# Kernel tuning notes

Hardware: AMD Instinct MI355X
Metric: run time of the kernel (lower is better)

The kernel has to match this reference:

```python
import jax, jax.numpy as jnp
import numpy as np
from jax import lax

B, N, C = 8, 16384, 128
HEADS, FF, KS = 8, 3.0, 5
HD = C // HEADS

def setup_inputs() -> dict:
    key = jax.random.key(0)
    ks = jax.random.split(key, 10)
    r = lambda k, s, sc=0.02: jax.random.normal(k, s, dtype=jnp.float32) * sc
    return {
        "x": jax.random.normal(ks[0], (B, N, C), dtype=jnp.float32),
        "Wq": r(ks[1], (C, C)),
        "Wkv": r(ks[2], (C, C)),
        "Wproj": r(ks[3], (C, C)),
        "bproj": jnp.zeros((C,), jnp.float32),
        "w_g": jax.random.normal(ks[4], (C, 1), dtype=jnp.float32),
        "scale": r(ks[5], (1, 1, C), 0.1),
        "pos_enc": r(ks[6], (1, N, C), 0.02),
        "dwc_w": r(ks[7], (HD, 1, KS, KS), 0.1),
        "dwc_b": jnp.zeros((HD,), jnp.float32),
        "H": 128,
        "W": 128,
    }

def _l2(a, axis):
    return jnp.sqrt(jnp.sum(a * a, axis=axis, keepdims=True))

def reference(x, Wq, Wkv, Wproj, bproj, w_g, scale, pos_enc, dwc_w, dwc_b, H, W):
    b, n_tok, c = x.shape
    scale_factor = HD ** (-0.5)
    q = x @ Wq.T                      # (B,N,C)
    k = x @ Wkv.T + pos_enc           # (B,N,C)  sr_ratio=1 path
    s = jax.nn.softplus(scale)
    q = (jax.nn.relu(q) + 1e-6) / s
    k = (jax.nn.relu(k) + 1e-6) / s
    qn, kn = _l2(q, -1), _l2(k, -1)
    q = q ** FF
    k = k ** FF
    q = q / _l2(q, -1) * qn
    k = k / _l2(k, -1) * kn
    A = (q @ w_g) * scale_factor      # (B,N,1)
    A = A / jnp.maximum(_l2(A, 1), 1e-12)  # F.normalize over dim=1
    G = jnp.sum(A * q, axis=1)        # (B,C)
    xg = G[:, None, :] * k            # (B,N,C)
    qh = q.reshape(b, n_tok, HEADS, HD).transpose(0, 2, 1, 3)  # (B,h,N,d)
    kh = k.reshape(b, n_tok, HEADS, HD).transpose(0, 2, 1, 3)
    z = 1.0 / (jnp.einsum('bhnd,bhd->bhn', qh, kh.mean(axis=2)) + 1e-6)
    xh = xg.reshape(b, n_tok, HEADS, HD).transpose(0, 2, 1, 3) * z[..., None]
    xo = xh.transpose(0, 2, 1, 3).reshape(b, n_tok, c)
    # faithful second transpose+reshape (memory reinterpretation in the source)
    xo = xo.transpose(0, 2, 1).reshape(b, n_tok, c)
    kimg = kh.reshape(b * HEADS, H, W, HD).transpose(0, 3, 1, 2)  # (B*h,d,H,W)
    pad = KS // 2
    conv = lax.conv_general_dilated(kimg, dwc_w, (1, 1), [(pad, pad), (pad, pad)],
                                    dimension_numbers=('NCHW', 'OIHW', 'NCHW'),
                                    feature_group_count=HD)
    conv = conv + dwc_b[None, :, None, None]
    xo = xo + conv.reshape(b, c, n_tok).transpose(0, 2, 1)
    return xo @ Wproj.T + bproj
```

## Files before the change

### kernel.cpp

```cpp
#include <hip/hip_runtime.h>
#include <hip/hip_bf16.h>

#define BB 8
#define NN 16384
#define CC 128

typedef __attribute__((ext_vector_type(8))) short bf16x8;
typedef __attribute__((ext_vector_type(4))) short short4v;
typedef __attribute__((ext_vector_type(4))) float f32x4;

__device__ __forceinline__ unsigned short f2bf(float f) {
    union { float f; unsigned u; } v; v.f = f;
    unsigned r = v.u + 0x7fffu + ((v.u >> 16) & 1u);
    return (unsigned short)(r >> 16);
}
__device__ __forceinline__ float bf2f(unsigned short h) {
    union { unsigned u; float f; } v; v.u = ((unsigned)h) << 16;
    return v.f;
}
__device__ __forceinline__ void split_trunc(float f, short& hi, short& lo) {
    union { float f; unsigned u; } v; v.f = f;
    const unsigned short hu = (unsigned short)(v.u >> 16);
    union { unsigned u; float f; } hf; hf.u = ((unsigned)hu) << 16;
    union { float f; unsigned u; } r; r.f = f - hf.f;
    hi = (short)hu;
    lo = (short)(r.u >> 16);
}

__global__ __launch_bounds__(256) void wprep_kernel(
    const float* __restrict__ Wq, const float* __restrict__ Wkv,
    const float* __restrict__ Wp, const float* __restrict__ scale,
    unsigned short* __restrict__ whi, unsigned short* __restrict__ wlo,
    float* __restrict__ sps)
{
    const int bid = blockIdx.x;
    if (bid == 48) {
        if (threadIdx.x < 128)
            sps[threadIdx.x] = 1.f / log1pf(expf(scale[threadIdx.x]));
        return;
    }
    const int mat = bid >> 4;
    const float* src = (mat == 0) ? Wq : ((mat == 1) ? Wkv : Wp);
    const int off = (bid & 15) * 1024 + threadIdx.x * 4;
    const float4 v = *(const float4*)(src + off);
    float f[4] = {v.x, v.y, v.z, v.w};
    short4v hv, lv;
#pragma unroll
    for (int j = 0; j < 4; ++j) {
        short h, lo2;
        split_trunc(f[j], h, lo2);
        hv[j] = h; lv[j] = lo2;
    }
    *(short4v*)(whi + mat * 16384 + off) = hv;
    *(short4v*)(wlo + mat * 16384 + off) = lv;
}

__global__ __launch_bounds__(256, 1) void qk_mfma_kernel(
    const float* __restrict__ x, const unsigned short* __restrict__ whi,
    const unsigned short* __restrict__ wlo, const float* __restrict__ w_g,
    const float* __restrict__ sps, const float* __restrict__ pos_enc,
    unsigned short* __restrict__ qout, unsigned short* __restrict__ ktout,
    float* __restrict__ partial)
{
    __shared__ __align__(16) char wsm[131072];
    __shared__ float wpart[4][257];
    __shared__ float apl[128];

    const int tid  = threadIdx.x;
    const int w    = tid >> 6;
    const int l    = tid & 63;
    const int blk  = blockIdx.x;
    const int tok0 = blk * 128;
    const int tokb = (blk & 127) * 128;

    bf16x8 xh[2][4], xl[2][4];
#pragma unroll
    for (int n = 0; n < 2; ++n) {
        const int r = w * 32 + n * 16 + (l & 15);
        const float* rowp = x + (tok0 + r) * 128 + (l >> 4) * 8;
#pragma unroll
        for (int kt = 0; kt < 4; ++kt) {
            const f32x4 a = *(const f32x4*)(rowp + kt * 32);
            const f32x4 b = *(const f32x4*)(rowp + kt * 32 + 4);
            const float f[8] = {a[0], a[1], a[2], a[3], b[0], b[1], b[2], b[3]};
            bf16x8 hv, lv;
#pragma unroll
            for (int j = 0; j < 8; ++j) {
                short h, lo2;
                split_trunc(f[j], h, lo2);
                hv[j] = h; lv[j] = lo2;
            }
            xh[n][kt] = hv; xl[n][kt] = lv;
        }
    }

#pragma unroll
    for (int it = 0; it < 32; ++it) {
        const int flat = it * 256 + tid;
        const int arr  = flat >> 11;
        const int c    = (flat >> 4) & 127;
        const int g    = flat & 15;
        const unsigned short* src = ((arr & 1) ? wlo : whi)
                                  + ((arr >> 1) ? 16384 : 0) + c * 128 + g * 8;
        const int dst = arr * 32768 + c * 256 + ((g * 16) ^ ((c & 7) << 4));
        *(bf16x8*)(wsm + dst) = *(const bf16x8*)src;
    }
    __syncthreads();

    const int crow = (l >> 4) * 4;
    f32x4 accq[8][2], acck[8][2];
#pragma unroll
    for (int m = 0; m < 8; ++m)
#pragma unroll
        for (int n = 0; n < 2; ++n) { accq[m][n] = (f32x4)0.f; acck[m][n] = (f32x4)0.f; }

#pragma unroll
    for (int m = 0; m < 8; ++m) {
        const int c = m * 16 + (l & 15);
        const int sw = (c & 7) << 4;
        bf16x8 aqh[4], aql[4], akh[4], akl[4];
#pragma unroll
        for (int kt = 0; kt < 4; ++kt) {
            const int fo = c * 256 + ((kt * 64 + (l >> 4) * 16) ^ sw);
            aqh[kt] = *(const bf16x8*)(wsm + fo);
            aql[kt] = *(const bf16x8*)(wsm + 32768 + fo);
            akh[kt] = *(const bf16x8*)(wsm + 65536 + fo);
            akl[kt] = *(const bf16x8*)(wsm + 98304 + fo);
        }
#pragma unroll
        for (int n = 0; n < 2; ++n)
#pragma unroll
            for (int kt = 0; kt < 4; ++kt) {
                accq[m][n] = __builtin_amdgcn_mfma_f32_16x16x32_bf16(aqh[kt], xh[n][kt], accq[m][n], 0, 0, 0);
                acck[m][n] = __builtin_amdgcn_mfma_f32_16x16x32_bf16(akh[kt], xh[n][kt], acck[m][n], 0, 0, 0);
                accq[m][n] = __builtin_amdgcn_mfma_f32_16x16x32_bf16(aqh[kt], xl[n][kt], accq[m][n], 0, 0, 0);
                acck[m][n] = __builtin_amdgcn_mfma_f32_16x16x32_bf16(akh[kt], xl[n][kt], acck[m][n], 0, 0, 0);
                accq[m][n] = __builtin_amdgcn_mfma_f32_16x16x32_bf16(aql[kt], xh[n][kt], accq[m][n], 0, 0, 0);
                acck[m][n] = __builtin_amdgcn_mfma_f32_16x16x32_bf16(akl[kt], xh[n][kt], acck[m][n], 0, 0, 0);
            }
    }
    __syncthreads();

    {
#pragma unroll
        for (int m = 0; m < 8; ++m) {
            const float4 is4 = *(const float4*)(sps + m * 16 + crow);
            const float is[4] = {is4.x, is4.y, is4.z, is4.w};
#pragma unroll
            for (int n = 0; n < 2; ++n)
#pragma unroll
                for (int j = 0; j < 4; ++j)
                    accq[m][n][j] = (fmaxf(accq[m][n][j], 0.f) + 1e-6f) * is[j];
        }
        float fqn[2];
#pragma unroll
        for (int n = 0; n < 2; ++n) {
            float s2 = 0.f, s6 = 0.f;
#pragma unroll
            for (int m = 0; m < 8; ++m)
#pragma unroll
                for (int j = 0; j < 4; ++j) {
                    const float v = accq[m][n][j], v2 = v * v;
                    s2 += v2; s6 += v2 * v2 * v2;
                }
            s2 += __shfl_xor(s2, 16); s6 += __shfl_xor(s6, 16);
            s2 += __shfl_xor(s2, 32); s6 += __shfl_xor(s6, 32);
            fqn[n] = sqrtf(s2 / s6);
        }
#pragma unroll
        for (int m = 0; m < 8; ++m)
#pragma unroll
            for (int n = 0; n < 2; ++n)
#pragma unroll
                for (int j = 0; j < 4; ++j) {
                    const float v = accq[m][n][j];
                    accq[m][n][j] = v * v * v * fqn[n];
                }
        float d0 = 0.f, d1 = 0.f;
#pragma unroll
        for (int m = 0; m < 8; ++m) {
            const float4 wgv = *(const float4*)(w_g + m * 16 + crow);
#pragma unroll
            for (int j = 0; j < 4; ++j) {
                const float wg = (j == 0) ? wgv.x : (j == 1) ? wgv.y : (j == 2) ? wgv.z : wgv.w;
                d0 += accq[m][0][j] * wg;
                d1 += accq[m][1][j] * wg;
            }
        }
        d0 += __shfl_xor(d0, 16); d0 += __shfl_xor(d0, 32);
        d1 += __shfl_xor(d1, 16); d1 += __shfl_xor(d1, 32);
        const float ap0 = 0.25f * d0, ap1 = 0.25f * d1;

        float ssa = ap0 * ap0 + ap1 * ap1;
        ssa += __shfl_xor(ssa, 1); ssa += __shfl_xor(ssa, 2);
        ssa += __shfl_xor(ssa, 4); ssa += __shfl_xor(ssa, 8);
        if (l == 0) wpart[w][256] = ssa;
        if (l < 16) { apl[w * 32 + l] = ap0; apl[w * 32 + 16 + l] = ap1; }

        float g4[4] = {0.f, 0.f, 0.f, 0.f};
#pragma unroll
        for (int n = 0; n < 2; ++n) {
            const int t = l & 15;
            const int rb = w * 8192 + t * 512;
#pragma unroll
            for (int m = 0; m < 8; ++m) {
                const int ad = rb + (((m * 16 + crow) * 4) ^ ((t & 7) << 4));
                *(f32x4*)(wsm + ad) = accq[m][n];
            }
            asm volatile("s_waitcnt lgkmcnt(0)" ::: "memory");
#pragma unroll
            for (int j = 0; j < 8; ++j) {
                const int fid = j * 64 + l;
                const int row = fid >> 5;
                const int c4  = fid & 31;
                const int rb3 = w * 8192 + row * 512;
                const f32x4 v = *(f32x4*)(wsm + rb3 + ((c4 * 16) ^ ((row & 7) << 4)));
                const float apv = apl[w * 32 + n * 16 + row];
                short4v qv;
#pragma unroll
                for (int i = 0; i < 4; ++i) {
                    g4[i] += apv * v[i];
                    qv[i] = (short)f2bf(v[i]);
                }
                *(short4v*)(qout + (tok0 + w * 32 + n * 16 + row) * 128 + c4 * 4) = qv;
            }
        }
#pragma unroll
        for (int i = 0; i < 4; ++i) g4[i] += __shfl_xor(g4[i], 32);
        if (l < 32) {
#pragma unroll
            for (int i = 0; i < 4; ++i) wpart[w][(l & 31) * 4 + i] = g4[i];
        }
    }

    {
#pragma unroll
        for (int m = 0; m < 8; ++m) {
            const float4 is4 = *(const float4*)(sps + m * 16 + crow);
            const float is[4] = {is4.x, is4.y, is4.z, is4.w};
#pragma unroll
            for (int n = 0; n < 2; ++n) {
                const int t = tokb + w * 32 + n * 16 + (l & 15);
                const float4 p = *(const float4*)(pos_enc + t * 128 + m * 16 + crow);
                const float pe[4] = {p.x, p.y, p.z, p.w};
#pragma unroll
                for (int j = 0; j < 4; ++j)
                    acck[m][n][j] = (fmaxf(acck[m][n][j] + pe[j], 0.f) + 1e-6f) * is[j];
            }
        }
        float fkn[2];
#pragma unroll
        for (int n = 0; n < 2; ++n) {
            float s2 = 0.f, s6 = 0.f;
#pragma unroll
            for (int m = 0; m < 8; ++m)
#pragma unroll
                for (int j = 0; j < 4; ++j) {
                    const float v = acck[m][n][j], v2 = v * v;
                    s2 += v2; s6 += v2 * v2 * v2;
                }
            s2 += __shfl_xor(s2, 16); s6 += __shfl_xor(s6, 16);
            s2 += __shfl_xor(s2, 32); s6 += __shfl_xor(s6, 32);
            fkn[n] = sqrtf(s2 / s6);
        }
#pragma unroll
        for (int m = 0; m < 8; ++m)
#pragma unroll
            for (int n = 0; n < 2; ++n)
#pragma unroll
                for (int j = 0; j < 4; ++j) {
                    const float v = acck[m][n][j];
                    acck[m][n][j] = v * v * v * fkn[n];
                }
#pragma unroll
        for (int m = 0; m < 8; ++m)
#pragma unroll
            for (int j = 0; j < 4; ++j) {
                float s = acck[m][0][j] + acck[m][1][j];
                s += __shfl_xor(s, 1); s += __shfl_xor(s, 2);
                s += __shfl_xor(s, 4); s += __shfl_xor(s, 8);
                if ((l & 15) == 0) wpart[w][128 + m * 16 + crow + j] = s;
            }
    }

    __syncthreads();
#pragma unroll
    for (int m = 0; m < 8; ++m)
#pragma unroll
        for (int n = 0; n < 2; ++n)
#pragma unroll
            for (int j = 0; j < 4; ++j) {
                const int ch = m * 16 + crow + j;
                const int tl = w * 32 + n * 16 + (l & 15);
                *(unsigned short*)(wsm + ch * 264 + tl * 2) = f2bf(acck[m][n][j]);
            }
    __syncthreads();
    {
        const int bb = blk >> 7;
        unsigned* ktp = (unsigned*)ktout;
#pragma unroll
        for (int it = 0; it < 32; ++it) {
            const int idx = it * 256 + tid;
            const int row = idx >> 6;
            const int col = idx & 63;
            const unsigned v = *(unsigned*)(wsm + row * 264 + col * 4);
            ktp[(size_t)(bb * 128 + row) * 8192 + (blk & 127) * 64 + col] = v;
        }
    }

    __syncthreads();
    float* pblk = partial + blk * 257;
    if (tid < 128) {
        pblk[tid] = wpart[0][tid] + wpart[1][tid] + wpart[2][tid] + wpart[3][tid];
        pblk[128 + tid] = wpart[0][128 + tid] + wpart[1][128 + tid] +
                          wpart[2][128 + tid] + wpart[3][128 + tid];
    } else if (tid == 128) {
        pblk[256] = wpart[0][256] + wpart[1][256] + wpart[2][256] + wpart[3][256];
    }
}

__global__ __launch_bounds__(256) void reduce_kernel(
    const float* __restrict__ partial, float* __restrict__ G,
    float* __restrict__ kbar)
{
    const int b = blockIdx.x;
    const int tid = threadIdx.x;
    __shared__ float tmp[4];

    float ssa = (tid < 128) ? partial[(b * 128 + tid) * 257 + 256] : 0.f;
#pragma unroll
    for (int o = 32; o >= 1; o >>= 1) ssa += __shfl_xor(ssa, o);
    if ((tid & 63) == 0) tmp[tid >> 6] = ssa;
    __syncthreads();
    const float anorm = fmaxf(sqrtf(tmp[0] + tmp[1] + tmp[2] + tmp[3]), 1e-12f);
    const float inv_a = 1.f / anorm;

    if (tid < 128) {
        float g = 0.f;
        for (int t = 0; t < 128; ++t)
            g += partial[(b * 128 + t) * 257 + tid];
        G[b * 128 + tid] = g * inv_a;
    } else {
        const int c2 = tid - 128;
        float s = 0.f;
        for (int t = 0; t < 128; ++t)
            s += partial[(b * 128 + t) * 257 + 128 + c2];
        kbar[b * 128 + c2] = s * (1.f / 16384.f);
    }
}

__global__ __launch_bounds__(256) void z_kernel(
    const unsigned short* __restrict__ q, const float* __restrict__ kbar,
    float* __restrict__ z)
{
    const int bid = blockIdx.x;
    const int b   = bid >> 8;
    const int tg  = bid & 255;
    const int tid = threadIdx.x;
    const int t   = tid >> 2;
    const int qt  = tid & 3;
    const int tok = tg * 64 + t;

    const unsigned short* qp = q + ((size_t)b * NN + tok) * 128 + qt * 32;
    const float* kb = kbar + b * 128 + qt * 32;

    float dot0 = 0.f, dot1 = 0.f;
#pragma unroll
    for (int c = 0; c < 4; ++c) {
        const short4v q4a = *(const short4v*)(qp + c * 8);
        const short4v q4b = *(const short4v*)(qp + c * 8 + 4);
        const float4 k4a = *(const float4*)(kb + c * 8);
        const float4 k4b = *(const float4*)(kb + c * 8 + 4);
        float d = bf2f((unsigned short)q4a[0]) * k4a.x + bf2f((unsigned short)q4a[1]) * k4a.y +
                  bf2f((unsigned short)q4a[2]) * k4a.z + bf2f((unsigned short)q4a[3]) * k4a.w +
                  bf2f((unsigned short)q4b[0]) * k4b.x + bf2f((unsigned short)q4b[1]) * k4b.y +
                  bf2f((unsigned short)q4b[2]) * k4b.z + bf2f((unsigned short)q4b[3]) * k4b.w;
        if (c < 2) dot0 += d; else dot1 += d;
    }
    z[((size_t)b * 8 + qt * 2) * NN + tok]     = 1.f / (dot0 + 1e-6f);
    z[((size_t)b * 8 + qt * 2 + 1) * NN + tok] = 1.f / (dot1 + 1e-6f);
}

__global__ __launch_bounds__(256, 2) void scp_kernel(
    float* __restrict__ out, const unsigned short* __restrict__ kt,
    const float* __restrict__ z, const float* __restrict__ G,
    const unsigned short* __restrict__ whi, const unsigned short* __restrict__ wlo,
    const float* __restrict__ bp, const float* __restrict__ dwc_w,
    const float* __restrict__ dwc_b)
{
    __shared__ __align__(16) char smem[32768];
    __shared__ float wct[25][16];
    __shared__ float bi[16];
    __shared__ float Gs;

    const int tid  = threadIdx.x;
    const int bid0 = blockIdx.x;
    const int bid  = (bid0 & 7) * 128 + (bid0 >> 3);
    const int cc   = bid & 127;
    const int b    = bid >> 7;
    const int n0   = bid * 128;

    for (int i = tid; i < 400; i += 256)
        wct[i >> 4][i & 15] = dwc_w[(i & 15) * 25 + (i >> 4)];
    if (tid < 16) bi[tid] = dwc_b[tid];
    if (tid == 0) Gs = G[b * 128 + cc];
    __syncthreads();

    const int ch4 = tid >> 3;
    const int xg  = tid & 7;

    float acc[4][16];
#pragma unroll
    for (int c = 0; c < 4; ++c)
#pragma unroll
        for (int i = 0; i < 16; ++i) acc[c][i] = 0.f;

#pragma unroll
    for (int dy = 0; dy < 5; ++dy) {
        const int yy = cc + dy - 2;
        if (yy < 0 || yy > 127) continue;
#pragma unroll
        for (int c = 0; c < 4; ++c) {
            const int ch = ch4 * 4 + c;
            const unsigned short* rowp = kt + ((size_t)b * 128 + ch) * NN
                                            + yy * 128 + xg * 16 - 8;
            float wf[32];
#pragma unroll
            for (int q4 = 0; q4 < 4; ++q4) {
                const bf16x8 v = *(const bf16x8*)(rowp + q4 * 8);
#pragma unroll
                for (int e = 0; e < 8; ++e)
                    wf[q4 * 8 + e] = bf2f((unsigned short)v[e]);
            }
            if (xg == 0) {
#pragma unroll
                for (int e = 0; e < 8; ++e) wf[e] = 0.f;
            }
            if (xg == 7) {
#pragma unroll
                for (int e = 24; e < 32; ++e) wf[e] = 0.f;
            }
            const int d = ch & 15;
#pragma unroll
            for (int dx = 0; dx < 5; ++dx) {
                const float wv = wct[dy * 5 + dx][d];
#pragma unroll
                for (int i = 0; i < 16; ++i)
                    acc[c][i] += wv * wf[i + dx + 6];
            }
        }
    }

    const float Gcc = Gs;
    const unsigned short* kub = kt + ((size_t)b * 128 + cc) * NN;
    const float* zr = z + ((size_t)b * 8 + (cc >> 4)) * NN;
    const int dbase = (ch4 & 3) * 4;
    const float4 b4 = *(const float4*)(&bi[dbase]);
    const float bv[4] = {b4.x, b4.y, b4.z, b4.w};
#pragma unroll
    for (int i = 0; i < 16; ++i) {
        const int r = xg * 16 + i;
        const int toks = r * 128 + ch4 * 4;
        const short4v ku4 = *(const short4v*)(kub + toks);
        const float4 z4 = *(const float4*)(zr + toks);
        const float zz[4] = {z4.x, z4.y, z4.z, z4.w};
        short4v hv;
#pragma unroll
        for (int c = 0; c < 4; ++c) {
            const float f = Gcc * bf2f((unsigned short)ku4[c]) * zz[c] + acc[c][i] + bv[c];
            hv[c] = (short)f2bf(f);
        }
        const int ad = r * 256 + (((ch4 >> 1) * 16) ^ ((r & 7) << 4)) + (ch4 & 1) * 8;
        *(short4v*)(smem + ad) = hv;
    }
    __syncthreads();

    const int w  = tid >> 6;
    const int ll = tid & 63;
    bf16x8 xh[2][4];
    {
        const int lg16 = (ll >> 4) * 16;
#pragma unroll
        for (int n = 0; n < 2; ++n) {
            const int r = w * 32 + n * 16 + (ll & 15);
            const int rb = r * 256;
            const int sw = (r & 7) << 4;
#pragma unroll
            for (int kt2 = 0; kt2 < 4; ++kt2)
                xh[n][kt2] = *(bf16x8*)(smem + rb + ((kt2 * 64 + lg16) ^ sw));
        }
    }
    const int crow = (ll >> 4) * 4;
    f32x4 pacc[8][2];
#pragma unroll
    for (int m = 0; m < 8; ++m)
#pragma unroll
        for (int n = 0; n < 2; ++n) pacc[m][n] = (f32x4)0.f;

#pragma unroll
    for (int m = 0; m < 8; ++m) {
        const int c = m * 16 + (ll & 15);
        bf16x8 ah[4], al[4];
#pragma unroll
        for (int kt2 = 0; kt2 < 4; ++kt2) {
            const int off = 32768 + c * 128 + kt2 * 32 + (ll >> 4) * 8;
            ah[kt2] = *(const bf16x8*)(whi + off);
            al[kt2] = *(const bf16x8*)(wlo + off);
        }
#pragma unroll
        for (int n = 0; n < 2; ++n)
#pragma unroll
            for (int kt2 = 0; kt2 < 4; ++kt2) {
                pacc[m][n] = __builtin_amdgcn_mfma_f32_16x16x32_bf16(ah[kt2], xh[n][kt2], pacc[m][n], 0, 0, 0);
                pacc[m][n] = __builtin_amdgcn_mfma_f32_16x16x32_bf16(al[kt2], xh[n][kt2], pacc[m][n], 0, 0, 0);
            }
    }

#pragma unroll
    for (int m = 0; m < 8; ++m) {
        const float4 bq = *(const float4*)(bp + m * 16 + crow);
        const float bb[4] = {bq.x, bq.y, bq.z, bq.w};
#pragma unroll
        for (int n = 0; n < 2; ++n)
#pragma unroll
            for (int j = 0; j < 4; ++j) pacc[m][n][j] += bb[j];
    }
    __syncthreads();
#pragma unroll
    for (int n = 0; n < 2; ++n) {
        const int t = ll & 15;
        const int rb = w * 8192 + t * 512;
#pragma unroll
        for (int m = 0; m < 8; ++m) {
            const int ad = rb + (((m * 16 + crow) * 4) ^ ((t & 7) << 4));
            *(f32x4*)(smem + ad) = pacc[m][n];
        }
        asm volatile("s_waitcnt lgkmcnt(0)" ::: "memory");
#pragma unroll
        for (int j = 0; j < 8; ++j) {
            const int fid = j * 64 + ll;
            const int row = fid >> 5;
            const int c4  = fid & 31;
            const int rb3 = w * 8192 + row * 512;
            const f32x4 v = *(f32x4*)(smem + rb3 + ((c4 * 16) ^ ((row & 7) << 4)));
            *(f32x4*)(out + (n0 + w * 32 + n * 16 + row) * 128 + c4 * 4) = v;
        }
    }
}

extern "C" void kernel_launch(void* const* d_in, const int* in_sizes, int n_in,
                              void* d_out, int out_size, void* d_ws, size_t ws_size,
                              hipStream_t stream)
{
    const float* x       = (const float*)d_in[0];
    const float* Wq      = (const float*)d_in[1];
    const float* Wkv     = (const float*)d_in[2];
    const float* Wproj   = (const float*)d_in[3];
    const float* bproj   = (const float*)d_in[4];
    const float* w_g     = (const float*)d_in[5];
    const float* scale   = (const float*)d_in[6];
    const float* pos_enc = (const float*)d_in[7];
    const float* dwc_w   = (const float*)d_in[8];
    const float* dwc_b   = (const float*)d_in[9];
    float* out = (float*)d_out;

    char* ws = (char*)d_ws;
    unsigned short* qbuf = (unsigned short*)(ws);
    unsigned short* ktbuf= (unsigned short*)(ws + 33554432);
    float* partial = (float*)(ws + 67108864);
    float* G       = (float*)(ws + 68161536);
    float* kbar    = (float*)(ws + 68165632);
    unsigned short* whi = (unsigned short*)(ws + 68169728);
    unsigned short* wlo = (unsigned short*)(ws + 68268032);
    float* sps     = (float*)(ws + 68366336);
    float* zbuf    = (float*)(ws + 68366848);

    wprep_kernel<<<dim3(49), dim3(256), 0, stream>>>(
        Wq, Wkv, Wproj, scale, whi, wlo, sps);
    qk_mfma_kernel<<<dim3(1024), dim3(256), 0, stream>>>(
        x, whi, wlo, w_g, sps, pos_enc, qbuf, ktbuf, partial);
    reduce_kernel<<<dim3(8), dim3(256), 0, stream>>>(partial, G, kbar);
    z_kernel<<<dim3(2048), dim3(256), 0, stream>>>(qbuf, kbar, zbuf);
    scp_kernel<<<dim3(1024), dim3(256), 0, stream>>>(
        out, ktbuf, zbuf, G, whi, wlo, bproj, dwc_w, dwc_b);
}
```

Baseline: 181.0 us.

## Split fused Q/K projection kernel into separate Q and K kernels

The single kernel that computed both Q and K projections, holding 128 KB of weights in LDS and two accumulator sets with one block per CU, is split into two kernels. Each loads only its own 64 KB of split-bf16 weights and has one accumulator set, and the launch bound allows two blocks per CU. The aim is higher occupancy and better latency hiding, at the price of reading and splitting x twice and paying an extra launch. The partial-sum buffers are separated and the reduce kernel is updated to match.

```diff
diff --git a/kernel.cpp b/kernel.cpp
--- a/kernel.cpp
+++ b/kernel.cpp
@@ -55,16 +55,189 @@
     *(short4v*)(wlo + mat * 16384 + off) = lv;
 }
 
-__global__ __launch_bounds__(256, 1) void qk_mfma_kernel(
+__global__ __launch_bounds__(256, 2) void qproj_kernel(
     const float* __restrict__ x, const unsigned short* __restrict__ whi,
     const unsigned short* __restrict__ wlo, const float* __restrict__ w_g,
+    const float* __restrict__ sps,
+    unsigned short* __restrict__ qout, float* __restrict__ partial1)
+{
+    __shared__ __align__(16) char wsm[65536];
+    __shared__ float wpart[4][132];
+    __shared__ float apl[128];
+
+    const int tid  = threadIdx.x;
+    const int w    = tid >> 6;
+    const int l    = tid & 63;
+    const int blk  = blockIdx.x;
+    const int tok0 = blk * 128;
+
+    bf16x8 xh[2][4], xl[2][4];
+#pragma unroll
+    for (int n = 0; n < 2; ++n) {
+        const int r = w * 32 + n * 16 + (l & 15);
+        const float* rowp = x + (tok0 + r) * 128 + (l >> 4) * 8;
+#pragma unroll
+        for (int kt = 0; kt < 4; ++kt) {
+            const f32x4 a = *(const f32x4*)(rowp + kt * 32);
+            const f32x4 b = *(const f32x4*)(rowp + kt * 32 + 4);
+            const float f[8] = {a[0], a[1], a[2], a[3], b[0], b[1], b[2], b[3]};
+            bf16x8 hv, lv;
+#pragma unroll
+            for (int j = 0; j < 8; ++j) {
+                short h, lo2;
+                split_trunc(f[j], h, lo2);
+                hv[j] = h; lv[j] = lo2;
+            }
+            xh[n][kt] = hv; xl[n][kt] = lv;
+        }
+    }
+
+#pragma unroll
+    for (int it = 0; it < 16; ++it) {
+        const int flat = it * 256 + tid;
+        const int arr  = flat >> 11;
+        const int c    = (flat >> 4) & 127;
+        const int g    = flat & 15;
+        const unsigned short* src = (arr ? wlo : whi) + c * 128 + g * 8;
+        const int dst = arr * 32768 + c * 256 + ((g * 16) ^ ((c & 7) << 4));
+        *(bf16x8*)(wsm + dst) = *(const bf16x8*)src;
+    }
+    __syncthreads();
+
+    const int crow = (l >> 4) * 4;
+    f32x4 acc[8][2];
+#pragma unroll
+    for (int m = 0; m < 8; ++m)
+#pragma unroll
+        for (int n = 0; n < 2; ++n) acc[m][n] = (f32x4)0.f;
+
+#pragma unroll
+    for (int m = 0; m < 8; ++m) {
+        const int c = m * 16 + (l & 15);
+        const int sw = (c & 7) << 4;
+        bf16x8 ah[4], al[4];
+#pragma unroll
+        for (int kt = 0; kt < 4; ++kt) {
+            const int fo = c * 256 + ((kt * 64 + (l >> 4) * 16) ^ sw);
+            ah[kt] = *(const bf16x8*)(wsm + fo);
+            al[kt] = *(const bf16x8*)(wsm + 32768 + fo);
+        }
+#pragma unroll
+        for (int n = 0; n < 2; ++n)
+#pragma unroll
+            for (int kt = 0; kt < 4; ++kt) {
+                acc[m][n] = __builtin_amdgcn_mfma_f32_16x16x32_bf16(ah[kt], xh[n][kt], acc[m][n], 0, 0, 0);
+                acc[m][n] = __builtin_amdgcn_mfma_f32_16x16x32_bf16(ah[kt], xl[n][kt], acc[m][n], 0, 0, 0);
+                acc[m][n] = __builtin_amdgcn_mfma_f32_16x16x32_bf16(al[kt], xh[n][kt], acc[m][n], 0, 0, 0);
+            }
+    }
+    __syncthreads();
+
+#pragma unroll
+    for (int m = 0; m < 8; ++m) {
+        const float4 is4 = *(const float4*)(sps + m * 16 + crow);
+        const float is[4] = {is4.x, is4.y, is4.z, is4.w};
+#pragma unroll
+        for (int n = 0; n < 2; ++n)
+#pragma unroll
+            for (int j = 0; j < 4; ++j)
+                acc[m][n][j] = (fmaxf(acc[m][n][j], 0.f) + 1e-6f) * is[j];
+    }
+    float fqn[2];
+#pragma unroll
+    for (int n = 0; n < 2; ++n) {
+        float s2 = 0.f, s6 = 0.f;
+#pragma unroll
+        for (int m = 0; m < 8; ++m)
+#pragma unroll
+            for (int j = 0; j < 4; ++j) {
+                const float v = acc[m][n][j], v2 = v * v;
+                s2 += v2; s6 += v2 * v2 * v2;
+            }
+        s2 += __shfl_xor(s2, 16); s6 += __shfl_xor(s6, 16);
+        s2 += __shfl_xor(s2, 32); s6 += __shfl_xor(s6, 32);
+        fqn[n] = sqrtf(s2 / s6);
+    }
+#pragma unroll
+    for (int m = 0; m < 8; ++m)
+#pragma unroll
+        for (int n = 0; n < 2; ++n)
+#pragma unroll
+            for (int j = 0; j < 4; ++j) {
+                const float v = acc[m][n][j];
+                acc[m][n][j] = v * v * v * fqn[n];
+            }
+    float d0 = 0.f, d1 = 0.f;
+#pragma unroll
+    for (int m = 0; m < 8; ++m) {
+        const float4 wgv = *(const float4*)(w_g + m * 16 + crow);
+#pragma unroll
+        for (int j = 0; j < 4; ++j) {
+            const float wg = (j == 0) ? wgv.x : (j == 1) ? wgv.y : (j == 2) ? wgv.z : wgv.w;
+            d0 += acc[m][0][j] * wg;
+            d1 += acc[m][1][j] * wg;
+        }
+    }
+    d0 += __shfl_xor(d0, 16); d0 += __shfl_xor(d0, 32);
+    d1 += __shfl_xor(d1, 16); d1 += __shfl_xor(d1, 32);
+    const float ap0 = 0.25f * d0, ap1 = 0.25f * d1;
+
+    float ssa = ap0 * ap0 + ap1 * ap1;
+    ssa += __shfl_xor(ssa, 1); ssa += __shfl_xor(ssa, 2);
+    ssa += __shfl_xor(ssa, 4); ssa += __shfl_xor(ssa, 8);
+    if (l == 0) wpart[w][128] = ssa;
+    if (l < 16) { apl[w * 32 + l] = ap0; apl[w * 32 + 16 + l] = ap1; }
+
+    float g4[4] = {0.f, 0.f, 0.f, 0.f};
+#pragma unroll
+    for (int n = 0; n < 2; ++n) {
+        const int t = l & 15;
+        const int rb = w * 8192 + t * 512;
+#pragma unroll
+        for (int m = 0; m < 8; ++m) {
+            const int ad = rb + (((m * 16 + crow) * 4) ^ ((t & 7) << 4));
+            *(f32x4*)(wsm + ad) = acc[m][n];
+        }
+        asm volatile("s_waitcnt lgkmcnt(0)" ::: "memory");
+#pragma unroll
+        for (int j = 0; j < 8; ++j) {
+            const int fid = j * 64 + l;
+            const int row = fid >> 5;
+            const int c4  = fid & 31;
+            const int rb3 = w * 8192 + row * 512;
+            const f32x4 v = *(f32x4*)(wsm + rb3 + ((c4 * 16) ^ ((row & 7) << 4)));
+            const float apv = apl[w * 32 + n * 16 + row];
+            short4v qv;
+#pragma unroll
+            for (int i = 0; i < 4; ++i) {
+                g4[i] += apv * v[i];
+                qv[i] = (short)f2bf(v[i]);
+            }
+            *(short4v*)(qout + (tok0 + w * 32 + n * 16 + row) * 128 + c4 * 4) = qv;
+        }
+    }
+#pragma unroll
+    for (int i = 0; i < 4; ++i) g4[i] += __shfl_xor(g4[i], 32);
+    if (l < 32) {
+#pragma unroll
+        for (int i = 0; i < 4; ++i) wpart[w][(l & 31) * 4 + i] = g4[i];
+    }
+    __syncthreads();
+    float* pblk = partial1 + blk * 132;
+    if (tid < 128)
+        pblk[tid] = wpart[0][tid] + wpart[1][tid] + wpart[2][tid] + wpart[3][tid];
+    else if (tid == 128)
+        pblk[128] = wpart[0][128] + wpart[1][128] + wpart[2][128] + wpart[3][128];
+}
+
+__global__ __launch_bounds__(256, 2) void kproj_kernel(
+    const float* __restrict__ x, const unsigned short* __restrict__ whi,
+    const unsigned short* __restrict__ wlo,
     const float* __restrict__ sps, const float* __restrict__ pos_enc,
-    unsigned short* __restrict__ qout, unsigned short* __restrict__ ktout,
-    float* __restrict__ partial)
+    unsigned short* __restrict__ ktout, float* __restrict__ partial2)
 {
-    __shared__ __align__(16) char wsm[131072];
-    __shared__ float wpart[4][257];
-    __shared__ float apl[128];
+    __shared__ __align__(16) char wsm[65536];
+    __shared__ float wpart[4][128];
 
     const int tid  = threadIdx.x;
     const int w    = tid >> 6;
@@ -95,195 +268,94 @@
     }
 
 #pragma unroll
-    for (int it = 0; it < 32; ++it) {
+    for (int it = 0; it < 16; ++it) {
         const int flat = it * 256 + tid;
         const int arr  = flat >> 11;
         const int c    = (flat >> 4) & 127;
         const int g    = flat & 15;
-        const unsigned short* src = ((arr & 1) ? wlo : whi)
-                                  + ((arr >> 1) ? 16384 : 0) + c * 128 + g * 8;
+        const unsigned short* src = (arr ? wlo : whi) + 16384 + c * 128 + g * 8;
         const int dst = arr * 32768 + c * 256 + ((g * 16) ^ ((c & 7) << 4));
         *(bf16x8*)(wsm + dst) = *(const bf16x8*)src;
     }
     __syncthreads();
 
     const int crow = (l >> 4) * 4;
-    f32x4 accq[8][2], acck[8][2];
+    f32x4 acc[8][2];
 #pragma unroll
     for (int m = 0; m < 8; ++m)
 #pragma unroll
-        for (int n = 0; n < 2; ++n) { accq[m][n] = (f32x4)0.f; acck[m][n] = (f32x4)0.f; }
+        for (int n = 0; n < 2; ++n) acc[m][n] = (f32x4)0.f;
 
 #pragma unroll
     for (int m = 0; m < 8; ++m) {
         const int c = m * 16 + (l & 15);
         const int sw = (c & 7) << 4;
-        bf16x8 aqh[4], aql[4], akh[4], akl[4];
+        bf16x8 ah[4], al[4];
 #pragma unroll
         for (int kt = 0; kt < 4; ++kt) {
             const int fo = c * 256 + ((kt * 64 + (l >> 4) * 16) ^ sw);
-            aqh[kt] = *(const bf16x8*)(wsm + fo);
-            aql[kt] = *(const bf16x8*)(wsm + 32768 + fo);
-            akh[kt] = *(const bf16x8*)(wsm + 65536 + fo);
-            akl[kt] = *(const bf16x8*)(wsm + 98304 + fo);
+            ah[kt] = *(const bf16x8*)(wsm + fo);
+            al[kt] = *(const bf16x8*)(wsm + 32768 + fo);
         }
 #pragma unroll
         for (int n = 0; n < 2; ++n)
 #pragma unroll
             for (int kt = 0; kt < 4; ++kt) {
-                accq[m][n] = __builtin_amdgcn_mfma_f32_16x16x32_bf16(aqh[kt], xh[n][kt], accq[m][n], 0, 0, 0);
-                acck[m][n] = __builtin_amdgcn_mfma_f32_16x16x32_bf16(akh[kt], xh[n][kt], acck[m][n], 0, 0, 0);
-                accq[m][n] = __builtin_amdgcn_mfma_f32_16x16x32_bf16(aqh[kt], xl[n][kt], accq[m][n], 0, 0, 0);
-                acck[m][n] = __builtin_amdgcn_mfma_f32_16x16x32_bf16(akh[kt], xl[n][kt], acck[m][n], 0, 0, 0);
-                accq[m][n] = __builtin_amdgcn_mfma_f32_16x16x32_bf16(aql[kt], xh[n][kt], accq[m][n], 0, 0, 0);
-                acck[m][n] = __builtin_amdgcn_mfma_f32_16x16x32_bf16(akl[kt], xh[n][kt], acck[m][n], 0, 0, 0);
-            }
-    }
-    __syncthreads();
-
-    {
-#pragma unroll
-        for (int m = 0; m < 8; ++m) {
-            const float4 is4 = *(const float4*)(sps + m * 16 + crow);
-            const float is[4] = {is4.x, is4.y, is4.z, is4.w};
-#pragma unroll
-            for (int n = 0; n < 2; ++n)
-#pragma unroll
-                for (int j = 0; j < 4; ++j)
-                    accq[m][n][j] = (fmaxf(accq[m][n][j], 0.f) + 1e-6f) * is[j];
-        }
-        float fqn[2];
+                acc[m][n] = __builtin_amdgcn_mfma_f32_16x16x32_bf16(ah[kt], xh[n][kt], acc[m][n], 0, 0, 0);
+                acc[m][n] = __builtin_amdgcn_mfma_f32_16x16x32_bf16(ah[kt], xl[n][kt], acc[m][n], 0, 0, 0);
+                acc[m][n] = __builtin_amdgcn_mfma_f32_16x16x32_bf16(al[kt], xh[n][kt], acc[m][n], 0, 0, 0);
+            }
+    }
+    __syncthreads();
+
+#pragma unroll
+    for (int m = 0; m < 8; ++m) {
+        const float4 is4 = *(const float4*)(sps + m * 16 + crow);
+        const float is[4] = {is4.x, is4.y, is4.z, is4.w};
 #pragma unroll
         for (int n = 0; n < 2; ++n) {
-            float s2 = 0.f, s6 = 0.f;
-#pragma unroll
-            for (int m = 0; m < 8; ++m)
-#pragma unroll
-                for (int j = 0; j < 4; ++j) {
-                    const float v = accq[m][n][j], v2 = v * v;
-                    s2 += v2; s6 += v2 * v2 * v2;
-                }
-            s2 += __shfl_xor(s2, 16); s6 += __shfl_xor(s6, 16);
-            s2 += __shfl_xor(s2, 32); s6 += __shfl_xor(s6, 32);
-            fqn[n] = sqrtf(s2 / s6);
-        }
+            const int t = tokb + w * 32 + n * 16 + (l & 15);
+            const float4 p = *(const float4*)(pos_enc + t * 128 + m * 16 + crow);
+            const float pe[4] = {p.x, p.y, p.z, p.w};
+#pragma unroll
+            for (int j = 0; j < 4; ++j)
+                acc[m][n][j] = (fmaxf(acc[m][n][j] + pe[j], 0.f) + 1e-6f) * is[j];
+        }
+    }
+    float fkn[2];
+#pragma unroll
+    for (int n = 0; n < 2; ++n) {
+        float s2 = 0.f, s6 = 0.f;
 #pragma unroll
         for (int m = 0; m < 8; ++m)
 #pragma unroll
-            for (int n = 0; n < 2; ++n)
-#pragma unroll
-                for (int j = 0; j < 4; ++j) {
-                    const float v = accq[m][n][j];
-                    accq[m][n][j] = v * v * v * fqn[n];
-                }
-        float d0 = 0.f, d1 = 0.f;
-#pragma unroll
-        for (int m = 0; m < 8; ++m) {
-            const float4 wgv = *(const float4*)(w_g + m * 16 + crow);
-#pragma unroll
             for (int j = 0; j < 4; ++j) {
-                const float wg = (j == 0) ? wgv.x : (j == 1) ? wgv.y : (j == 2) ? wgv.z : wgv.w;
-                d0 += accq[m][0][j] * wg;
-                d1 += accq[m][1][j] * wg;
-            }
-        }
-        d0 += __shfl_xor(d0, 16); d0 += __shfl_xor(d0, 32);
-        d1 += __shfl_xor(d1, 16); d1 += __shfl_xor(d1, 32);
-        const float ap0 = 0.25f * d0, ap1 = 0.25f * d1;
-
-        float ssa = ap0 * ap0 + ap1 * ap1;
-        ssa += __shfl_xor(ssa, 1); ssa += __shfl_xor(ssa, 2);
-        ssa += __shfl_xor(ssa, 4); ssa += __shfl_xor(ssa, 8);
-        if (l == 0) wpart[w][256] = ssa;
-        if (l < 16) { apl[w * 32 + l] = ap0; apl[w * 32 + 16 + l] = ap1; }
-
-        float g4[4] = {0.f, 0.f, 0.f, 0.f};
-#pragma unroll
-        for (int n = 0; n < 2; ++n) {
-            const int t = l & 15;
-            const int rb = w * 8192 + t * 512;
-#pragma unroll
-            for (int m = 0; m < 8; ++m) {
-                const int ad = rb + (((m * 16 + crow) * 4) ^ ((t & 7) << 4));
-                *(f32x4*)(wsm + ad) = accq[m][n];
-            }
-            asm volatile("s_waitcnt lgkmcnt(0)" ::: "memory");
-#pragma unroll
-            for (int j = 0; j < 8; ++j) {
-                const int fid = j * 64 + l;
-                const int row = fid >> 5;
-                const int c4  = fid & 31;
-                const int rb3 = w * 8192 + row * 512;
-                const f32x4 v = *(f32x4*)(wsm + rb3 + ((c4 * 16) ^ ((row & 7) << 4)));
-                const float apv = apl[w * 32 + n * 16 + row];
-                short4v qv;
-#pragma unroll
-                for (int i = 0; i < 4; ++i) {
-                    g4[i] += apv * v[i];
-                    qv[i] = (short)f2bf(v[i]);
-                }
-                *(short4v*)(qout + (tok0 + w * 32 + n * 16 + row) * 128 + c4 * 4) = qv;
-            }
-        }
-#pragma unroll
-        for (int i = 0; i < 4; ++i) g4[i] += __shfl_xor(g4[i], 32);
-        if (l < 32) {
-#pragma unroll
-            for (int i = 0; i < 4; ++i) wpart[w][(l & 31) * 4 + i] = g4[i];
-        }
-    }
-
-    {
-#pragma unroll
-        for (int m = 0; m < 8; ++m) {
-            const float4 is4 = *(const float4*)(sps + m * 16 + crow);
-            const float is[4] = {is4.x, is4.y, is4.z, is4.w};
-#pragma unroll
-            for (int n = 0; n < 2; ++n) {
-                const int t = tokb + w * 32 + n * 16 + (l & 15);
-                const float4 p = *(const float4*)(pos_enc + t * 128 + m * 16 + crow);
-                const float pe[4] = {p.x, p.y, p.z, p.w};
-#pragma unroll
-                for (int j = 0; j < 4; ++j)
-                    acck[m][n][j] = (fmaxf(acck[m][n][j] + pe[j], 0.f) + 1e-6f) * is[j];
-            }
-        }
-        float fkn[2];
-#pragma unroll
-        for (int n = 0; n < 2; ++n) {
-            float s2 = 0.f, s6 = 0.f;
-#pragma unroll
-            for (int m = 0; m < 8; ++m)
-#pragma unroll
-                for (int j = 0; j < 4; ++j) {
-                    const float v = acck[m][n][j], v2 = v * v;
-                    s2 += v2; s6 += v2 * v2 * v2;
-                }
-            s2 += __shfl_xor(s2, 16); s6 += __shfl_xor(s6, 16);
-            s2 += __shfl_xor(s2, 32); s6 += __shfl_xor(s6, 32);
-            fkn[n] = sqrtf(s2 / s6);
-        }
-#pragma unroll
-        for (int m = 0; m < 8; ++m)
-#pragma unroll
-            for (int n = 0; n < 2; ++n)
-#pragma unroll
-                for (int j = 0; j < 4; ++j) {
-                    const float v = acck[m][n][j];
-                    acck[m][n][j] = v * v * v * fkn[n];
-                }
-#pragma unroll
-        for (int m = 0; m < 8; ++m)
+                const float v = acc[m][n][j], v2 = v * v;
+                s2 += v2; s6 += v2 * v2 * v2;
+            }
+        s2 += __shfl_xor(s2, 16); s6 += __shfl_xor(s6, 16);
+        s2 += __shfl_xor(s2, 32); s6 += __shfl_xor(s6, 32);
+        fkn[n] = sqrtf(s2 / s6);
+    }
+#pragma unroll
+    for (int m = 0; m < 8; ++m)
+#pragma unroll
+        for (int n = 0; n < 2; ++n)
 #pragma unroll
             for (int j = 0; j < 4; ++j) {
-                float s = acck[m][0][j] + acck[m][1][j];
-                s += __shfl_xor(s, 1); s += __shfl_xor(s, 2);
-                s += __shfl_xor(s, 4); s += __shfl_xor(s, 8);
-                if ((l & 15) == 0) wpart[w][128 + m * 16 + crow + j] = s;
-            }
-    }
-
-    __syncthreads();
+                const float v = acc[m][n][j];
+                acc[m][n][j] = v * v * v * fkn[n];
+            }
+#pragma unroll
+    for (int m = 0; m < 8; ++m)
+#pragma unroll
+        for (int j = 0; j < 4; ++j) {
+            float s = acc[m][0][j] + acc[m][1][j];
+            s += __shfl_xor(s, 1); s += __shfl_xor(s, 2);
+            s += __shfl_xor(s, 4); s += __shfl_xor(s, 8);
+            if ((l & 15) == 0) wpart[w][m * 16 + crow + j] = s;
+        }
+
 #pragma unroll
     for (int m = 0; m < 8; ++m)
 #pragma unroll
@@ -292,7 +364,7 @@
             for (int j = 0; j < 4; ++j) {
                 const int ch = m * 16 + crow + j;
                 const int tl = w * 32 + n * 16 + (l & 15);
-                *(unsigned short*)(wsm + ch * 264 + tl * 2) = f2bf(acck[m][n][j]);
+                *(unsigned short*)(wsm + ch * 264 + tl * 2) = f2bf(acc[m][n][j]);
             }
     __syncthreads();
     {
@@ -307,27 +379,21 @@
             ktp[(size_t)(bb * 128 + row) * 8192 + (blk & 127) * 64 + col] = v;
         }
     }
-
-    __syncthreads();
-    float* pblk = partial + blk * 257;
-    if (tid < 128) {
-        pblk[tid] = wpart[0][tid] + wpart[1][tid] + wpart[2][tid] + wpart[3][tid];
-        pblk[128 + tid] = wpart[0][128 + tid] + wpart[1][128 + tid] +
-                          wpart[2][128 + tid] + wpart[3][128 + tid];
-    } else if (tid == 128) {
-        pblk[256] = wpart[0][256] + wpart[1][256] + wpart[2][256] + wpart[3][256];
-    }
+    __syncthreads();
+    if (tid < 128)
+        partial2[blk * 128 + tid] = wpart[0][tid] + wpart[1][tid] +
+                                    wpart[2][tid] + wpart[3][tid];
 }
 
 __global__ __launch_bounds__(256) void reduce_kernel(
-    const float* __restrict__ partial, float* __restrict__ G,
-    float* __restrict__ kbar)
+    const float* __restrict__ partial1, const float* __restrict__ partial2,
+    float* __restrict__ G, float* __restrict__ kbar)
 {
     const int b = blockIdx.x;
     const int tid = threadIdx.x;
     __shared__ float tmp[4];
 
-    float ssa = (tid < 128) ? partial[(b * 128 + tid) * 257 + 256] : 0.f;
+    float ssa = (tid < 128) ? partial1[(b * 128 + tid) * 132 + 128] : 0.f;
 #pragma unroll
     for (int o = 32; o >= 1; o >>= 1) ssa += __shfl_xor(ssa, o);
     if ((tid & 63) == 0) tmp[tid >> 6] = ssa;
@@ -338,13 +404,13 @@
     if (tid < 128) {
         float g = 0.f;
         for (int t = 0; t < 128; ++t)
-            g += partial[(b * 128 + t) * 257 + tid];
+            g += partial1[(b * 128 + t) * 132 + tid];
         G[b * 128 + tid] = g * inv_a;
     } else {
         const int c2 = tid - 128;
         float s = 0.f;
         for (int t = 0; t < 128; ++t)
-            s += partial[(b * 128 + t) * 257 + 128 + c2];
+            s += partial2[(b * 128 + t) * 128 + c2];
         kbar[b * 128 + c2] = s * (1.f / 16384.f);
     }
 }
@@ -567,19 +633,23 @@
     char* ws = (char*)d_ws;
     unsigned short* qbuf = (unsigned short*)(ws);
     unsigned short* ktbuf= (unsigned short*)(ws + 33554432);
-    float* partial = (float*)(ws + 67108864);
-    float* G       = (float*)(ws + 68161536);
-    float* kbar    = (float*)(ws + 68165632);
-    unsigned short* whi = (unsigned short*)(ws + 68169728);
-    unsigned short* wlo = (unsigned short*)(ws + 68268032);
-    float* sps     = (float*)(ws + 68366336);
-    float* zbuf    = (float*)(ws + 68366848);
+    float* partial1 = (float*)(ws + 67108864);
+    float* partial2 = (float*)(ws + 67649536);
+    float* G        = (float*)(ws + 68173824);
+    float* kbar     = (float*)(ws + 68177920);
+    unsigned short* whi = (unsigned short*)(ws + 68182016);
+    unsigned short* wlo = (unsigned short*)(ws + 68280320);
+    float* sps      = (float*)(ws + 68378624);
+    float* zbuf     = (float*)(ws + 68379136);
 
     wprep_kernel<<<dim3(49), dim3(256), 0, stream>>>(
         Wq, Wkv, Wproj, scale, whi, wlo, sps);
-    qk_mfma_kernel<<<dim3(1024), dim3(256), 0, stream>>>(
-        x, whi, wlo, w_g, sps, pos_enc, qbuf, ktbuf, partial);
-    reduce_kernel<<<dim3(8), dim3(256), 0, stream>>>(partial, G, kbar);
+    qproj_kernel<<<dim3(1024), dim3(256), 0, stream>>>(
+        x, whi, wlo, w_g, sps, qbuf, partial1);
+    kproj_kernel<<<dim3(1024), dim3(256), 0, stream>>>(
+        x, whi, wlo, sps, pos_enc, ktbuf, partial2);
+    reduce_kernel<<<dim3(8), dim3(256), 0, stream>>>(
+        partial1, partial2, G, kbar);
     z_kernel<<<dim3(2048), dim3(256), 0, stream>>>(qbuf, kbar, zbuf);
     scp_kernel<<<dim3(1024), dim3(256), 0, stream>>>(
         out, ktbuf, zbuf, G, whi, wlo, bproj, dwc_w, dwc_b);
```

New measurement: 169.4 us. 6.4% less time.
